# Kernel optimization log

Hardware: AMD Instinct MI355X
Metric: run time of the kernel (lower is better)

## Reference

```python
import jax, jax.numpy as jnp
import numpy as np

D_MODEL = 1024
NHEAD = 16
HEAD_DIM = D_MODEL // NHEAD


def setup_inputs() -> dict:
    key = jax.random.key(0)
    ks = jax.random.split(key, 11)
    B, S = 2, 2048
    scale = 1.0 / np.sqrt(D_MODEL)
    inp = {
        "query": jax.random.normal(ks[0], (B, S, D_MODEL), jnp.float32),
        "key": jax.random.normal(ks[1], (B, S, D_MODEL), jnp.float32),
        "value": jax.random.normal(ks[2], (B, S, D_MODEL), jnp.float32),
        "Wq": jax.random.normal(ks[3], (D_MODEL, D_MODEL), jnp.float32) * scale,
        "bq": jnp.zeros((D_MODEL,), jnp.float32),
        "Wk": jax.random.normal(ks[4], (D_MODEL, D_MODEL), jnp.float32) * scale,
        "bk": jnp.zeros((D_MODEL,), jnp.float32),
        "Wv": jax.random.normal(ks[5], (D_MODEL, D_MODEL), jnp.float32) * scale,
        "bv": jnp.zeros((D_MODEL,), jnp.float32),
        "Wo": jax.random.normal(ks[6], (D_MODEL, D_MODEL), jnp.float32) * scale,
        "bo": jnp.zeros((D_MODEL,), jnp.float32),
    }
    return inp


def reference(query, key, value, Wq, bq, Wk, bk, Wv, bv, Wo, bo):
    B, S, _ = query.shape
    # Linear projections (torch Linear: x @ W.T + b)
    def proj(x, W, b):
        y = x @ W.T + b
        return y.reshape(B, -1, NHEAD, HEAD_DIM).transpose(0, 2, 1, 3)  # [B,H,S,hd]
    q = proj(query, Wq, bq)
    k = proj(key, Wk, bk)
    v = proj(value, Wv, bv)
    scores = jnp.einsum("bhqd,bhkd->bhqk", q, k) / np.sqrt(HEAD_DIM)
    attn = jax.nn.softmax(scores, axis=-1)  # dropout is identity (eval / p=0)
    out = jnp.einsum("bhqk,bhkd->bhqd", attn, v)
    out = out.transpose(0, 2, 1, 3).reshape(B, S, D_MODEL)
    return out @ Wo.T + bo
```

## Files before the change

### kernel.cpp

```cpp
#include <hip/hip_runtime.h>
#include <stdint.h>

typedef __attribute__((ext_vector_type(8))) short bf16x8;
typedef __attribute__((ext_vector_type(4))) short bf16x4;
typedef __attribute__((ext_vector_type(4))) float f32x4;
typedef __attribute__((ext_vector_type(2))) unsigned int u32x2;
typedef unsigned int u32;
typedef unsigned short u16;

#define S_LEN 2048
#define DMODEL 1024
#define HD 64


static __device__ __forceinline__ u16 f2bf(float f) {
  u32 u = __builtin_bit_cast(u32, f);
  return (u16)((u + 0x7fffu + ((u >> 16) & 1u)) >> 16);
}

static __device__ __forceinline__ u32 cvt_pk(float a, float b) {
  u32 r;
  asm("v_cvt_pk_bf16_f32 %0, %1, %2" : "=v"(r) : "v"(a), "v"(b));
  return r;
}

static __device__ __forceinline__ void gl_lds16(const u16* g, u16* l) {
  __builtin_amdgcn_global_load_lds((const __attribute__((address_space(1))) u32*)g,
                                   (__attribute__((address_space(3))) u32*)l, 16, 0, 0);
}

static __device__ __forceinline__ u32 lds_addr(const void* p) {
  return (u32)(uint64_t)p;
}

static __device__ __forceinline__ bf16x4 tr16(u32 addr) {
  bf16x4 r;
  asm volatile("ds_read_b64_tr_b16 %0, %1" : "=v"(r) : "v"(addr));
  return r;
}

__global__ __launch_bounds__(256) void convert_all(
    const float* __restrict__ xq, const float* __restrict__ xk, const float* __restrict__ xv,
    const float* __restrict__ wq, const float* __restrict__ wk,
    const float* __restrict__ wv, const float* __restrict__ wo,
    u16* __restrict__ dst) {
  size_t i = ((size_t)blockIdx.x * 256 + threadIdx.x) * 8;
  const float* src;
  size_t off;
  u32 t = (u32)(i >> 22);
  if (t < 3) {
    src = (t == 0) ? xq : (t == 1) ? xk : xv;
    off = i & 0x3FFFFFu;
  } else {
    u32 wsel = (u32)((i >> 20) & 3u);
    src = (wsel == 0) ? wq : (wsel == 1) ? wk : (wsel == 2) ? wv : wo;
    off = i & 0xFFFFFu;
  }
  float4 a = *(const float4*)(src + off);
  float4 b = *(const float4*)(src + off + 4);
  bf16x8 o;
  o[0] = (short)f2bf(a.x); o[1] = (short)f2bf(a.y);
  o[2] = (short)f2bf(a.z); o[3] = (short)f2bf(a.w);
  o[4] = (short)f2bf(b.x); o[5] = (short)f2bf(b.y);
  o[6] = (short)f2bf(b.z); o[7] = (short)f2bf(b.w);
  *(bf16x8*)(dst + i) = o;
}

template <int OUT_BF16, int BN>
static __device__ __forceinline__ void gemm_core(
    const u16* __restrict__ A, const u16* __restrict__ Bm,
    const float* __restrict__ bias, void* __restrict__ Y, float scale,
    int bm, int bn, u16* As, u16* Bs) {
  const int tid = threadIdx.x;
  const int lane = tid & 63, w = tid >> 6;
  const int wm = w >> 1, wn = w & 1;
  const int g = lane >> 4, l15 = lane & 15;
  constexpr int NFR = BN / 64 * 2;

  f32x4 acc[4][NFR] = {};

  const int r0 = tid >> 2, k8 = (tid & 3) * 8;
  const int r1 = (tid + 256) >> 2;
  const size_t arow0 = (size_t)(bm * 128 + r0) * DMODEL + k8;
  const size_t arow1 = (size_t)(bm * 128 + r1) * DMODEL + k8;
  const size_t brow0 = (size_t)(bn * BN + r0) * DMODEL + k8;
  const size_t brow1 = (size_t)(bn * BN + r1) * DMODEL + k8;

  auto stage = [&](int buf, int kt) {
    const int kb = kt * 32;
    u16* asb = As + buf * 4096;
    u16* bsb = Bs + buf * (BN * 32);
    gl_lds16(A + arow0 + kb, asb + w * 512);
    gl_lds16(A + arow1 + kb, asb + w * 512 + 2048);
    gl_lds16(Bm + brow0 + kb, bsb + w * 512);
    if constexpr (BN == 128) gl_lds16(Bm + brow1 + kb, bsb + w * 512 + 2048);
  };

  stage(0, 0);
  __syncthreads();
  int cur = 0;
  for (int kt = 0; kt < 32; ++kt) {
    if (kt < 31) stage(cur ^ 1, kt + 1);
    const u16* as = As + cur * 4096;
    const u16* bs = Bs + cur * (BN * 32);
    bf16x8 a[4], b[NFR];
#pragma unroll
    for (int mi = 0; mi < 4; ++mi)
      a[mi] = *(const bf16x8*)&as[(wm * 64 + mi * 16 + l15) * 32 + g * 8];
#pragma unroll
    for (int ni = 0; ni < NFR; ++ni)
      b[ni] = *(const bf16x8*)&bs[(wn * (BN / 2) + ni * 16 + l15) * 32 + g * 8];
#pragma unroll
    for (int mi = 0; mi < 4; ++mi)
#pragma unroll
      for (int ni = 0; ni < NFR; ++ni)
        acc[mi][ni] = __builtin_amdgcn_mfma_f32_16x16x32_bf16(a[mi], b[ni], acc[mi][ni], 0, 0, 0);
    __syncthreads();
    cur ^= 1;
  }

#pragma unroll
  for (int ni = 0; ni < NFR; ++ni) {
    const int col = bn * BN + wn * (BN / 2) + ni * 16 + l15;
    const float bv = bias[col];
#pragma unroll
    for (int mi = 0; mi < 4; ++mi) {
      const int row0 = bm * 128 + wm * 64 + mi * 16 + g * 4;
#pragma unroll
      for (int r = 0; r < 4; ++r) {
        float v = (acc[mi][ni][r] + bv) * scale;
        if (OUT_BF16)
          ((u16*)Y)[(size_t)(row0 + r) * DMODEL + col] = f2bf(v);
        else
          ((float*)Y)[(size_t)(row0 + r) * DMODEL + col] = v;
      }
    }
  }
}

__global__ __launch_bounds__(256) void qkv_gemm(
    const u16* __restrict__ X, const u16* __restrict__ W,
    const float* __restrict__ bq, const float* __restrict__ bk, const float* __restrict__ bv,
    u16* __restrict__ Qp, u16* __restrict__ Kpp, u16* __restrict__ Vpp, float qscale) {
  __shared__ u16 As[2 * 4096];
  __shared__ u16 Bs[2 * 4096];
  const int sel = blockIdx.x >> 8;
  const int bb = blockIdx.x & 255;
  const int bm = bb >> 3, bn = bb & 7;
  const size_t MB4 = 4096ull * 1024ull;
  const u16* A = X + (size_t)sel * MB4;
  const u16* Bmat = W + (size_t)sel * (1024 * 1024);
  const float* bias = (sel == 0) ? bq : (sel == 1) ? bk : bv;
  u16* Y = (sel == 0) ? Qp : (sel == 1) ? Kpp : Vpp;
  const float scale = (sel == 0) ? qscale : 1.0f;
  gemm_core<1, 128>(A, Bmat, bias, Y, scale, bm, bn, As, Bs);
}

__global__ __launch_bounds__(256) void wo_gemm(
    const u16* __restrict__ A, const u16* __restrict__ Bm,
    const float* __restrict__ bias, float* __restrict__ Y) {
  __shared__ u16 As[2 * 4096];
  __shared__ u16 Bs[2 * 2048];
  const int bm = blockIdx.x >> 4, bn = blockIdx.x & 15;
  gemm_core<0, 64>(A, Bm, bias, Y, 1.0f, bm, bn, As, Bs);
}

__global__ __launch_bounds__(512) void attn_fwd(
    const u16* __restrict__ Qp, const u16* __restrict__ Kp,
    const u16* __restrict__ Vp, u16* __restrict__ Op) {
  __shared__ u16 Kl[2 * 4096];
  __shared__ u16 Vl[2 * 4096];
  __shared__ u16 Pl[8 * 16 * 64];
  const int tid = threadIdx.x;
  const int lane = tid & 63, w = tid >> 6;
  const int g = lane >> 4, l15 = lane & 15;
  const int bh = blockIdx.x >> 4;
  const int qt = blockIdx.x & 15;
  const int b = bh >> 4, h = bh & 15;
  const size_t rowbase = (size_t)b * S_LEN;
  const int hcol = h * HD;

  const int qrow = qt * 128 + w * 16 + l15;
  const bf16x8 qf0 = *(const bf16x8*)(Qp + (rowbase + qrow) * DMODEL + hcol + g * 8);
  const bf16x8 qf1 = *(const bf16x8*)(Qp + (rowbase + qrow) * DMODEL + hcol + 32 + g * 8);

  f32x4 o[4] = {};
  float lsum = 0.0f;

  const u32 vb = lds_addr(Vl);

  const int kvA = tid >> 3, slA = (tid & 7) ^ (kvA & 7);
  const size_t koffA = (rowbase + kvA) * (size_t)DMODEL + hcol + slA * 8;
  const size_t voffA = [&] {
    int e = tid * 8;
    int hh = (e >> 3) & 1, p = (e >> 4) & 15, sub = (e >> 8) & 1;
    int dt = (e >> 9) & 3, blk = (e >> 11) & 1;
    int kv = blk * 32 + 8 * (p >> 2) + sub * 4 + (p & 3);
    return (rowbase + kv) * (size_t)DMODEL + hcol + dt * 16 + hh * 8;
  }();

  auto stage = [&](int buf, int kv0) {
    const size_t adv = (size_t)kv0 * DMODEL;
    gl_lds16(Kp + koffA + adv, Kl + buf * 4096 + w * 512);
    gl_lds16(Vp + voffA + adv, Vl + buf * 4096 + w * 512);
  };

  stage(0, 0);
  __syncthreads();
  int cur = 0;
  for (int it = 0; it < 32; ++it) {
    if (it < 31) stage(cur ^ 1, (it + 1) * 64);
    const char* kbase = (const char*)Kl + cur * 8192;

    f32x4 s[4];
    __builtin_amdgcn_s_setprio(1);
#pragma unroll
    for (int t = 0; t < 4; ++t) {
      const int kvl = t * 16 + l15;
      const u32 swz = (u32)((kvl & 7) << 4);
      bf16x8 k0 = *(const bf16x8*)(kbase + (((u32)(kvl * 128 + g * 16)) ^ swz));
      bf16x8 k1 = *(const bf16x8*)(kbase + (((u32)(kvl * 128 + 64 + g * 16)) ^ swz));
      f32x4 z = {};
      f32x4 acc0 = __builtin_amdgcn_mfma_f32_16x16x32_bf16(k0, qf0, z, 0, 0, 0);
      s[t] = __builtin_amdgcn_mfma_f32_16x16x32_bf16(k1, qf1, acc0, 0, 0, 0);
    }
    __builtin_amdgcn_s_setprio(0);

    float pvv[16];
    float psum = 0.0f;
#pragma unroll
    for (int t = 0; t < 4; ++t)
#pragma unroll
      for (int r = 0; r < 4; ++r) {
        float e = __builtin_amdgcn_exp2f(s[t][r]);
        pvv[t * 4 + r] = e;
        psum += e;
      }
    lsum += psum;

    const u32 pb = (u32)(w * 2048 + l15 * 128);
    const u32 pswz = (u32)((l15 & 7) << 4);
#pragma unroll
    for (int t = 0; t < 4; ++t) {
      u32x2 pk = {cvt_pk(pvv[t * 4 + 0], pvv[t * 4 + 1]),
                  cvt_pk(pvv[t * 4 + 2], pvv[t * 4 + 3])};
      *(u32x2*)((char*)Pl + ((pb + (u32)(t * 32 + g * 8)) ^ pswz)) = pk;
    }

    bf16x8 pf[2];
    bf16x4 tv[2][4][2];
    const u32 vbb = vb + (u32)(cur * 8192);
#pragma unroll
    for (int blk = 0; blk < 2; ++blk) {
      pf[blk] = *(const bf16x8*)((const char*)Pl + ((pb + (u32)(blk * 64 + g * 16)) ^ pswz));
#pragma unroll
      for (int dt = 0; dt < 4; ++dt)
#pragma unroll
        for (int sub = 0; sub < 2; ++sub)
          tv[blk][dt][sub] = tr16(vbb + (u32)((blk * 8 + dt * 2 + sub) * 512 + lane * 8));
    }
    asm volatile("s_waitcnt lgkmcnt(0)" ::: "memory");
    __builtin_amdgcn_sched_barrier(0);
    __builtin_amdgcn_s_setprio(1);
#pragma unroll
    for (int blk = 0; blk < 2; ++blk)
#pragma unroll
      for (int dt = 0; dt < 4; ++dt) {
        bf16x8 vf;
        vf[0] = tv[blk][dt][0][0]; vf[1] = tv[blk][dt][0][1];
        vf[2] = tv[blk][dt][0][2]; vf[3] = tv[blk][dt][0][3];
        vf[4] = tv[blk][dt][1][0]; vf[5] = tv[blk][dt][1][1];
        vf[6] = tv[blk][dt][1][2]; vf[7] = tv[blk][dt][1][3];
        o[dt] = __builtin_amdgcn_mfma_f32_16x16x32_bf16(pf[blk], vf, o[dt], 0, 0, 0);
      }
    __builtin_amdgcn_s_setprio(0);
    __syncthreads();
    cur ^= 1;
  }

  lsum += __shfl_xor(lsum, 16);
  lsum += __shfl_xor(lsum, 32);
  const float linv = 1.0f / lsum;
  const float li0 = __shfl(linv, g * 4 + 0);
  const float li1 = __shfl(linv, g * 4 + 1);
  const float li2 = __shfl(linv, g * 4 + 2);
  const float li3 = __shfl(linv, g * 4 + 3);
  const float li[4] = {li0, li1, li2, li3};
#pragma unroll
  for (int dt = 0; dt < 4; ++dt)
#pragma unroll
    for (int r = 0; r < 4; ++r) {
      const int qr = qt * 128 + w * 16 + g * 4 + r;
      Op[(rowbase + qr) * DMODEL + hcol + dt * 16 + l15] = f2bf(o[dt][r] * li[r]);
    }
}

extern "C" void kernel_launch(void* const* d_in, const int* in_sizes, int n_in,
                              void* d_out, int out_size, void* d_ws, size_t ws_size,
                              hipStream_t stream) {
  const float* xq = (const float*)d_in[0];
  const float* xk = (const float*)d_in[1];
  const float* xv = (const float*)d_in[2];
  const float* Wq = (const float*)d_in[3];
  const float* bq = (const float*)d_in[4];
  const float* Wk = (const float*)d_in[5];
  const float* bk = (const float*)d_in[6];
  const float* Wv = (const float*)d_in[7];
  const float* bv = (const float*)d_in[8];
  const float* Wo = (const float*)d_in[9];
  const float* bo = (const float*)d_in[10];

  u16* ws = (u16*)d_ws;
  const size_t MB4 = 4096ull * 1024ull;
  u16* XQ = ws;
  u16* WQb = ws + 3 * MB4;
  u16* Qp = ws + 4 * MB4;
  u16* Kpp = ws + 5 * MB4;
  u16* Vpp = ws + 6 * MB4;
  u16* Opp = ws + 7 * MB4;

  convert_all<<<8192, 256, 0, stream>>>(xq, xk, xv, Wq, Wk, Wv, Wo, ws);

  const float qscale = 0.125f * 1.44269504088896340736f;
  qkv_gemm<<<768, 256, 0, stream>>>(XQ, WQb, bq, bk, bv, Qp, Kpp, Vpp, qscale);

  attn_fwd<<<512, 512, 0, stream>>>(Qp, Kpp, Vpp, Opp);

  wo_gemm<<<512, 256, 0, stream>>>(Opp, WQb + 3 * 1024 * 1024, bo, (float*)d_out);
}
```

Before: 129.3 us.

## Process two query sub-tiles per wave in attention with half the threads

The attention kernel drops from 8 to 4 waves per block, and each wave now handles 32 query rows as two 16-row sub-tiles. Each K and V fragment read from LDS is reused across two MFMA accumulations, and every thread stages two chunks of K and V per iteration. The aim is fewer LDS reads and less sync overhead per unit of compute. The cost is more registers per wave and less latency hiding from having fewer waves per block.

```diff
diff --git a/kernel.cpp b/kernel.cpp
--- a/kernel.cpp
+++ b/kernel.cpp
@@ -165,7 +165,7 @@
   gemm_core<0, 64>(A, Bm, bias, Y, 1.0f, bm, bn, As, Bs);
 }
 
-__global__ __launch_bounds__(512) void attn_fwd(
+__global__ __launch_bounds__(256) void attn_fwd(
     const u16* __restrict__ Qp, const u16* __restrict__ Kp,
     const u16* __restrict__ Vp, u16* __restrict__ Op) {
   __shared__ u16 Kl[2 * 4096];
@@ -180,29 +180,38 @@
   const size_t rowbase = (size_t)b * S_LEN;
   const int hcol = h * HD;
 
-  const int qrow = qt * 128 + w * 16 + l15;
-  const bf16x8 qf0 = *(const bf16x8*)(Qp + (rowbase + qrow) * DMODEL + hcol + g * 8);
-  const bf16x8 qf1 = *(const bf16x8*)(Qp + (rowbase + qrow) * DMODEL + hcol + 32 + g * 8);
-
-  f32x4 o[4] = {};
-  float lsum = 0.0f;
+  bf16x8 qf[2][2];
+#pragma unroll
+  for (int qb = 0; qb < 2; ++qb) {
+    const int qrow = qt * 128 + w * 32 + qb * 16 + l15;
+    qf[qb][0] = *(const bf16x8*)(Qp + (rowbase + qrow) * DMODEL + hcol + g * 8);
+    qf[qb][1] = *(const bf16x8*)(Qp + (rowbase + qrow) * DMODEL + hcol + 32 + g * 8);
+  }
+
+  f32x4 o[2][4] = {};
+  float lsum[2] = {0.0f, 0.0f};
 
   const u32 vb = lds_addr(Vl);
 
   const int kvA = tid >> 3, slA = (tid & 7) ^ (kvA & 7);
+  const int kvB = (tid + 256) >> 3, slB = (tid & 7) ^ (kvB & 7);
   const size_t koffA = (rowbase + kvA) * (size_t)DMODEL + hcol + slA * 8;
-  const size_t voffA = [&] {
-    int e = tid * 8;
+  const size_t koffB = (rowbase + kvB) * (size_t)DMODEL + hcol + slB * 8;
+  auto vsrc = [&](int ch) {
+    int e = ch * 8;
     int hh = (e >> 3) & 1, p = (e >> 4) & 15, sub = (e >> 8) & 1;
     int dt = (e >> 9) & 3, blk = (e >> 11) & 1;
     int kv = blk * 32 + 8 * (p >> 2) + sub * 4 + (p & 3);
     return (rowbase + kv) * (size_t)DMODEL + hcol + dt * 16 + hh * 8;
-  }();
+  };
+  const size_t voffA = vsrc(tid), voffB = vsrc(tid + 256);
 
   auto stage = [&](int buf, int kv0) {
     const size_t adv = (size_t)kv0 * DMODEL;
     gl_lds16(Kp + koffA + adv, Kl + buf * 4096 + w * 512);
+    gl_lds16(Kp + koffB + adv, Kl + buf * 4096 + w * 512 + 2048);
     gl_lds16(Vp + voffA + adv, Vl + buf * 4096 + w * 512);
+    gl_lds16(Vp + voffB + adv, Vl + buf * 4096 + w * 512 + 2048);
   };
 
   stage(0, 0);
@@ -212,7 +221,7 @@
     if (it < 31) stage(cur ^ 1, (it + 1) * 64);
     const char* kbase = (const char*)Kl + cur * 8192;
 
-    f32x4 s[4];
+    f32x4 s[2][4];
     __builtin_amdgcn_s_setprio(1);
 #pragma unroll
     for (int t = 0; t < 4; ++t) {
@@ -221,44 +230,48 @@
       bf16x8 k0 = *(const bf16x8*)(kbase + (((u32)(kvl * 128 + g * 16)) ^ swz));
       bf16x8 k1 = *(const bf16x8*)(kbase + (((u32)(kvl * 128 + 64 + g * 16)) ^ swz));
       f32x4 z = {};
-      f32x4 acc0 = __builtin_amdgcn_mfma_f32_16x16x32_bf16(k0, qf0, z, 0, 0, 0);
-      s[t] = __builtin_amdgcn_mfma_f32_16x16x32_bf16(k1, qf1, acc0, 0, 0, 0);
+      s[0][t] = __builtin_amdgcn_mfma_f32_16x16x32_bf16(
+          k1, qf[0][1], __builtin_amdgcn_mfma_f32_16x16x32_bf16(k0, qf[0][0], z, 0, 0, 0), 0, 0, 0);
+      s[1][t] = __builtin_amdgcn_mfma_f32_16x16x32_bf16(
+          k1, qf[1][1], __builtin_amdgcn_mfma_f32_16x16x32_bf16(k0, qf[1][0], z, 0, 0, 0), 0, 0, 0);
     }
     __builtin_amdgcn_s_setprio(0);
 
-    float pvv[16];
-    float psum = 0.0f;
-#pragma unroll
-    for (int t = 0; t < 4; ++t)
-#pragma unroll
-      for (int r = 0; r < 4; ++r) {
-        float e = __builtin_amdgcn_exp2f(s[t][r]);
-        pvv[t * 4 + r] = e;
-        psum += e;
+    const u32 pswz = (u32)((l15 & 7) << 4);
+#pragma unroll
+    for (int qb = 0; qb < 2; ++qb) {
+      const u32 pb = (u32)((w * 2 + qb) * 2048 + l15 * 128);
+      float psum = 0.0f;
+#pragma unroll
+      for (int t = 0; t < 4; ++t) {
+        float e0 = __builtin_amdgcn_exp2f(s[qb][t][0]);
+        float e1 = __builtin_amdgcn_exp2f(s[qb][t][1]);
+        float e2 = __builtin_amdgcn_exp2f(s[qb][t][2]);
+        float e3 = __builtin_amdgcn_exp2f(s[qb][t][3]);
+        psum += (e0 + e1) + (e2 + e3);
+        u32x2 pk = {cvt_pk(e0, e1), cvt_pk(e2, e3)};
+        *(u32x2*)((char*)Pl + ((pb + (u32)(t * 32 + g * 8)) ^ pswz)) = pk;
       }
-    lsum += psum;
-
-    const u32 pb = (u32)(w * 2048 + l15 * 128);
-    const u32 pswz = (u32)((l15 & 7) << 4);
-#pragma unroll
-    for (int t = 0; t < 4; ++t) {
-      u32x2 pk = {cvt_pk(pvv[t * 4 + 0], pvv[t * 4 + 1]),
-                  cvt_pk(pvv[t * 4 + 2], pvv[t * 4 + 3])};
-      *(u32x2*)((char*)Pl + ((pb + (u32)(t * 32 + g * 8)) ^ pswz)) = pk;
+      lsum[qb] += psum;
     }
 
-    bf16x8 pf[2];
+    bf16x8 pf[2][2];
     bf16x4 tv[2][4][2];
     const u32 vbb = vb + (u32)(cur * 8192);
 #pragma unroll
-    for (int blk = 0; blk < 2; ++blk) {
-      pf[blk] = *(const bf16x8*)((const char*)Pl + ((pb + (u32)(blk * 64 + g * 16)) ^ pswz));
+    for (int qb = 0; qb < 2; ++qb) {
+      const u32 pb = (u32)((w * 2 + qb) * 2048 + l15 * 128);
+#pragma unroll
+      for (int blk = 0; blk < 2; ++blk)
+        pf[qb][blk] = *(const bf16x8*)((const char*)Pl + ((pb + (u32)(blk * 64 + g * 16)) ^ pswz));
+    }
+#pragma unroll
+    for (int blk = 0; blk < 2; ++blk)
 #pragma unroll
       for (int dt = 0; dt < 4; ++dt)
 #pragma unroll
         for (int sub = 0; sub < 2; ++sub)
           tv[blk][dt][sub] = tr16(vbb + (u32)((blk * 8 + dt * 2 + sub) * 512 + lane * 8));
-    }
     asm volatile("s_waitcnt lgkmcnt(0)" ::: "memory");
     __builtin_amdgcn_sched_barrier(0);
     __builtin_amdgcn_s_setprio(1);
@@ -271,28 +284,33 @@
         vf[2] = tv[blk][dt][0][2]; vf[3] = tv[blk][dt][0][3];
         vf[4] = tv[blk][dt][1][0]; vf[5] = tv[blk][dt][1][1];
         vf[6] = tv[blk][dt][1][2]; vf[7] = tv[blk][dt][1][3];
-        o[dt] = __builtin_amdgcn_mfma_f32_16x16x32_bf16(pf[blk], vf, o[dt], 0, 0, 0);
+        o[0][dt] = __builtin_amdgcn_mfma_f32_16x16x32_bf16(pf[0][blk], vf, o[0][dt], 0, 0, 0);
+        o[1][dt] = __builtin_amdgcn_mfma_f32_16x16x32_bf16(pf[1][blk], vf, o[1][dt], 0, 0, 0);
       }
     __builtin_amdgcn_s_setprio(0);
     __syncthreads();
     cur ^= 1;
   }
 
-  lsum += __shfl_xor(lsum, 16);
-  lsum += __shfl_xor(lsum, 32);
-  const float linv = 1.0f / lsum;
-  const float li0 = __shfl(linv, g * 4 + 0);
-  const float li1 = __shfl(linv, g * 4 + 1);
-  const float li2 = __shfl(linv, g * 4 + 2);
-  const float li3 = __shfl(linv, g * 4 + 3);
-  const float li[4] = {li0, li1, li2, li3};
-#pragma unroll
-  for (int dt = 0; dt < 4; ++dt)
-#pragma unroll
-    for (int r = 0; r < 4; ++r) {
-      const int qr = qt * 128 + w * 16 + g * 4 + r;
-      Op[(rowbase + qr) * DMODEL + hcol + dt * 16 + l15] = f2bf(o[dt][r] * li[r]);
-    }
+#pragma unroll
+  for (int qb = 0; qb < 2; ++qb) {
+    float ls = lsum[qb];
+    ls += __shfl_xor(ls, 16);
+    ls += __shfl_xor(ls, 32);
+    const float linv = 1.0f / ls;
+    const float li0 = __shfl(linv, g * 4 + 0);
+    const float li1 = __shfl(linv, g * 4 + 1);
+    const float li2 = __shfl(linv, g * 4 + 2);
+    const float li3 = __shfl(linv, g * 4 + 3);
+    const float li[4] = {li0, li1, li2, li3};
+#pragma unroll
+    for (int dt = 0; dt < 4; ++dt)
+#pragma unroll
+      for (int r = 0; r < 4; ++r) {
+        const int qr = qt * 128 + w * 32 + qb * 16 + g * 4 + r;
+        Op[(rowbase + qr) * DMODEL + hcol + dt * 16 + l15] = f2bf(o[qb][dt][r] * li[r]);
+      }
+  }
 }
 
 extern "C" void kernel_launch(void* const* d_in, const int* in_sizes, int n_in,
@@ -324,7 +342,7 @@
   const float qscale = 0.125f * 1.44269504088896340736f;
   qkv_gemm<<<768, 256, 0, stream>>>(XQ, WQb, bq, bk, bv, Qp, Kpp, Vpp, qscale);
 
-  attn_fwd<<<512, 512, 0, stream>>>(Qp, Kpp, Vpp, Opp);
+  attn_fwd<<<512, 256, 0, stream>>>(Qp, Kpp, Vpp, Opp);
 
   wo_gemm<<<512, 256, 0, stream>>>(Opp, WQb + 3 * 1024 * 1024, bo, (float*)d_out);
 }
```

Measured after the change: 134.1 us. +3.7%, slower.

## Fuse fp32-to-bf16 activation conversion into QKV GEMM A-tile loading

Applied to the files above, without the earlier changes.

The separate conversion pass over the query, key and value activations is removed. The QKV GEMM now loads fp32 A tiles straight from global memory into registers, packs them to bf16 with v_cvt_pk_bf16_f32 and writes them to LDS, while B still streams through global_load_lds. The goal is to skip writing and re-reading the 24MB bf16 activation copy. In exchange, each A tile is fetched as fp32 (twice the bytes, re-read by the 8 column blocks) and the register-staged A path may overlap less well with compute.

```diff
diff --git a/kernel.cpp b/kernel.cpp
--- a/kernel.cpp
+++ b/kernel.cpp
@@ -5,6 +5,7 @@
 typedef __attribute__((ext_vector_type(4))) short bf16x4;
 typedef __attribute__((ext_vector_type(4))) float f32x4;
 typedef __attribute__((ext_vector_type(2))) unsigned int u32x2;
+typedef __attribute__((ext_vector_type(4))) unsigned int u32x4;
 typedef unsigned int u32;
 typedef unsigned short u16;
 
@@ -39,23 +40,14 @@
   return r;
 }
 
-__global__ __launch_bounds__(256) void convert_all(
-    const float* __restrict__ xq, const float* __restrict__ xk, const float* __restrict__ xv,
+__global__ __launch_bounds__(256) void convert_w(
     const float* __restrict__ wq, const float* __restrict__ wk,
     const float* __restrict__ wv, const float* __restrict__ wo,
     u16* __restrict__ dst) {
   size_t i = ((size_t)blockIdx.x * 256 + threadIdx.x) * 8;
-  const float* src;
-  size_t off;
-  u32 t = (u32)(i >> 22);
-  if (t < 3) {
-    src = (t == 0) ? xq : (t == 1) ? xk : xv;
-    off = i & 0x3FFFFFu;
-  } else {
-    u32 wsel = (u32)((i >> 20) & 3u);
-    src = (wsel == 0) ? wq : (wsel == 1) ? wk : (wsel == 2) ? wv : wo;
-    off = i & 0xFFFFFu;
-  }
+  u32 wsel = (u32)((i >> 20) & 3u);
+  const float* src = (wsel == 0) ? wq : (wsel == 1) ? wk : (wsel == 2) ? wv : wo;
+  size_t off = i & 0xFFFFFu;
   float4 a = *(const float4*)(src + off);
   float4 b = *(const float4*)(src + off + 4);
   bf16x8 o;
@@ -139,7 +131,8 @@
 }
 
 __global__ __launch_bounds__(256) void qkv_gemm(
-    const u16* __restrict__ X, const u16* __restrict__ W,
+    const float* __restrict__ xq, const float* __restrict__ xk, const float* __restrict__ xv,
+    const u16* __restrict__ W,
     const float* __restrict__ bq, const float* __restrict__ bk, const float* __restrict__ bv,
     u16* __restrict__ Qp, u16* __restrict__ Kpp, u16* __restrict__ Vpp, float qscale) {
   __shared__ u16 As[2 * 4096];
@@ -147,13 +140,93 @@
   const int sel = blockIdx.x >> 8;
   const int bb = blockIdx.x & 255;
   const int bm = bb >> 3, bn = bb & 7;
-  const size_t MB4 = 4096ull * 1024ull;
-  const u16* A = X + (size_t)sel * MB4;
-  const u16* Bmat = W + (size_t)sel * (1024 * 1024);
+  const float* A = (sel == 0) ? xq : (sel == 1) ? xk : xv;
+  const u16* Bm = W + (size_t)sel * (1024 * 1024);
   const float* bias = (sel == 0) ? bq : (sel == 1) ? bk : bv;
   u16* Y = (sel == 0) ? Qp : (sel == 1) ? Kpp : Vpp;
   const float scale = (sel == 0) ? qscale : 1.0f;
-  gemm_core<1, 128>(A, Bmat, bias, Y, scale, bm, bn, As, Bs);
+
+  const int tid = threadIdx.x;
+  const int lane = tid & 63, w = tid >> 6;
+  const int wm = w >> 1, wn = w & 1;
+  const int g = lane >> 4, l15 = lane & 15;
+
+  f32x4 acc[4][4] = {};
+
+  const int r0 = tid >> 2, k8 = (tid & 3) * 8;
+  const int r1 = (tid + 256) >> 2;
+  const size_t arow0 = (size_t)(bm * 128 + r0) * DMODEL + k8;
+  const size_t arow1 = (size_t)(bm * 128 + r1) * DMODEL + k8;
+  const size_t brow0 = (size_t)(bn * 128 + r0) * DMODEL + k8;
+  const size_t brow1 = (size_t)(bn * 128 + r1) * DMODEL + k8;
+
+  float4 af0, af1, af2, af3;
+  auto loadA = [&](int kt) {
+    const int kb = kt * 32;
+    af0 = *(const float4*)(A + arow0 + kb);
+    af1 = *(const float4*)(A + arow0 + kb + 4);
+    af2 = *(const float4*)(A + arow1 + kb);
+    af3 = *(const float4*)(A + arow1 + kb + 4);
+  };
+  auto writeA = [&](int buf) {
+    u16* asb = As + buf * 4096;
+    u32x4 p0 = {cvt_pk(af0.x, af0.y), cvt_pk(af0.z, af0.w),
+                cvt_pk(af1.x, af1.y), cvt_pk(af1.z, af1.w)};
+    u32x4 p1 = {cvt_pk(af2.x, af2.y), cvt_pk(af2.z, af2.w),
+                cvt_pk(af3.x, af3.y), cvt_pk(af3.z, af3.w)};
+    *(u32x4*)(asb + tid * 8) = p0;
+    *(u32x4*)(asb + tid * 8 + 2048) = p1;
+  };
+  auto stageB = [&](int buf, int kt) {
+    const int kb = kt * 32;
+    u16* bsb = Bs + buf * 4096;
+    gl_lds16(Bm + brow0 + kb, bsb + w * 512);
+    gl_lds16(Bm + brow1 + kb, bsb + w * 512 + 2048);
+  };
+
+  loadA(0);
+  stageB(0, 0);
+  writeA(0);
+  __syncthreads();
+  int cur = 0;
+  for (int kt = 0; kt < 32; ++kt) {
+    if (kt < 31) {
+      loadA(kt + 1);
+      stageB(cur ^ 1, kt + 1);
+    }
+    const u16* as = As + cur * 4096;
+    const u16* bs = Bs + cur * 4096;
+    bf16x8 a[4], b[4];
+#pragma unroll
+    for (int mi = 0; mi < 4; ++mi)
+      a[mi] = *(const bf16x8*)&as[(wm * 64 + mi * 16 + l15) * 32 + g * 8];
+#pragma unroll
+    for (int ni = 0; ni < 4; ++ni)
+      b[ni] = *(const bf16x8*)&bs[(wn * 64 + ni * 16 + l15) * 32 + g * 8];
+#pragma unroll
+    for (int mi = 0; mi < 4; ++mi)
+#pragma unroll
+      for (int ni = 0; ni < 4; ++ni)
+        acc[mi][ni] = __builtin_amdgcn_mfma_f32_16x16x32_bf16(a[mi], b[ni], acc[mi][ni], 0, 0, 0);
+    if (kt < 31) writeA(cur ^ 1);
+    __syncthreads();
+    cur ^= 1;
+  }
+
+#pragma unroll
+  for (int ni = 0; ni < 4; ++ni) {
+    const int col = bn * 128 + wn * 64 + ni * 16 + l15;
+    const float bv = bias[col];
+#pragma unroll
+    for (int mi = 0; mi < 4; ++mi) {
+      const int row0 = bm * 128 + wm * 64 + mi * 16 + g * 4;
+#pragma unroll
+      for (int r = 0; r < 4; ++r) {
+        float v = (acc[mi][ni][r] + bv) * scale;
+        ((u16*)Y)[(size_t)(row0 + r) * DMODEL + col] = f2bf(v);
+      }
+    }
+  }
 }
 
 __global__ __launch_bounds__(256) void wo_gemm(
@@ -312,17 +385,16 @@
 
   u16* ws = (u16*)d_ws;
   const size_t MB4 = 4096ull * 1024ull;
-  u16* XQ = ws;
   u16* WQb = ws + 3 * MB4;
   u16* Qp = ws + 4 * MB4;
   u16* Kpp = ws + 5 * MB4;
   u16* Vpp = ws + 6 * MB4;
   u16* Opp = ws + 7 * MB4;
 
-  convert_all<<<8192, 256, 0, stream>>>(xq, xk, xv, Wq, Wk, Wv, Wo, ws);
+  convert_w<<<2048, 256, 0, stream>>>(Wq, Wk, Wv, Wo, WQb);
 
   const float qscale = 0.125f * 1.44269504088896340736f;
-  qkv_gemm<<<768, 256, 0, stream>>>(XQ, WQb, bq, bk, bv, Qp, Kpp, Vpp, qscale);
+  qkv_gemm<<<768, 256, 0, stream>>>(xq, xk, xv, WQb, bq, bk, bv, Qp, Kpp, Vpp, qscale);
 
   attn_fwd<<<512, 512, 0, stream>>>(Qp, Kpp, Vpp, Opp);
 
```

Result: slower. 141.5 us (+9.4%).
